# Performance work log

Hardware: AMD Instinct MI355X
Metric: run time of the kernel (lower is better)

Reference implementation:

```python
import jax, jax.numpy as jnp
import numpy as np

J = 1.0          # coupling constant
PT_PERIOD = 4    # parallel-tempering exchange every PT_PERIOD sweeps


def setup_inputs() -> dict:
    key = jax.random.key(0)
    k1, k2 = jax.random.split(key)
    B, C, L = 32, 16, 256
    # temperatures across the Ising critical region, sorted ascending
    T = jnp.sort(1.5 + 2.0 * jax.random.uniform(k1, (B,), dtype=jnp.float32))
    # spins stored as {0,1} ints; converted to +/-1 inside reference
    spins = jax.random.randint(k2, (B, C, L, L), 0, 2).astype(jnp.int32)
    return {"T": T, "spins": spins, "n_sweeps": 16}


def _neighbor_sum(s):
    # periodic 4-neighbor sum, shape preserved [B,C,L,L]
    return (jnp.roll(s, 1, -1) + jnp.roll(s, -1, -1)
            + jnp.roll(s, 1, -2) + jnp.roll(s, -1, -2))


def _energy(s):
    # total Ising energy per chain: -J * sum_<ij> s_i s_j  -> [B, C]
    return -J * jnp.sum(s * (jnp.roll(s, -1, -1) + jnp.roll(s, -1, -2)), axis=(-1, -2))


def reference(T, spins, n_sweeps):
    B, C, L, _ = spins.shape
    s = spins.astype(jnp.float32) * 2.0 - 1.0          # +/-1 spins
    ii = jnp.arange(L)
    parity = (ii[:, None] + ii[None, :]) % 2            # [L,L] checkerboard
    Tb = T[:, None, None, None]                         # [B,1,1,1]
    beta = 1.0 / T                                      # [B]
    base_key = jax.random.key(42)

    def half_sweep(s, key, color):
        dE = 2.0 * J * s * _neighbor_sum(s)             # local energy change on flip
        u = jax.random.uniform(key, s.shape, dtype=jnp.float32)
        acc = u < jnp.exp(-dE / Tb)                     # Metropolis accept
        mask = (parity == color)                        # update one sub-lattice only
        return jnp.where(mask & acc, -s, s)

    def pt_swap(s, key, pair_parity):
        # attempt swaps between adjacent temperatures (b, b+1) with given pair parity
        E = _energy(s)                                  # [B, C]
        d = (beta[:-1] - beta[1:])[:, None] * (E[:-1] - E[1:])   # [B-1, C]
        u = jax.random.uniform(key, (B - 1, C), dtype=jnp.float32)
        pair_mask = (jnp.arange(B - 1) % 2) == pair_parity
        acc = (u < jnp.exp(d)) & pair_mask[:, None]     # [B-1, C] non-overlapping
        swap_next = jnp.concatenate([acc, jnp.zeros((1, C), bool)], 0)  # swap b<->b+1
        swap_prev = jnp.concatenate([jnp.zeros((1, C), bool), acc], 0)
        s_next = jnp.roll(s, -1, axis=0)
        s_prev = jnp.roll(s, 1, axis=0)
        swn = swap_next[:, :, None, None]
        swp = swap_prev[:, :, None, None]
        return jnp.where(swn, s_next, jnp.where(swp, s_prev, s))

    def sweep(s, t):
        kb = jax.random.fold_in(base_key, t)
        k1, k2, k3 = jax.random.split(kb, 3)
        s = half_sweep(s, k1, 0)   # black sub-lattice
        s = half_sweep(s, k2, 1)   # white sub-lattice
        do_pt = (t % PT_PERIOD) == (PT_PERIOD - 1)
        s = jax.lax.cond(do_pt,
                         lambda s_: pt_swap(s_, k3, (t // PT_PERIOD) % 2),
                         lambda s_: s_, s)
        return s, None

    s, _ = jax.lax.scan(sweep, s, jnp.arange(n_sweeps))
    return s, _energy(s)
```

## Files before the change

### kernel.cpp

```cpp
#include <hip/hip_runtime.h>
#include <stdint.h>


#define BB 32
#define CC 16
#define PLANE 65536
#define NSITE (BB * CC * PLANE)
#define NPAIR ((BB - 1) * CC)
#define HSTRIP 64
#define ROWS_LD 69

__host__ __device__ __forceinline__ void tf2x32(uint32_t k0, uint32_t k1,
                                                uint32_t c0, uint32_t c1,
                                                uint32_t& o0, uint32_t& o1) {
  uint32_t ks2 = k0 ^ k1 ^ 0x1BD11BDAu;
  uint32_t x0 = c0 + k0;
  uint32_t x1 = c1 + k1;
#define TF_ROT(r) { x0 += x1; x1 = (x1 << (r)) | (x1 >> (32 - (r))); x1 ^= x0; }
  TF_ROT(13) TF_ROT(15) TF_ROT(26) TF_ROT(6)
  x0 += k1;  x1 += ks2 + 1u;
  TF_ROT(17) TF_ROT(29) TF_ROT(16) TF_ROT(24)
  x0 += ks2; x1 += k0 + 2u;
  TF_ROT(13) TF_ROT(15) TF_ROT(26) TF_ROT(6)
  x0 += k0;  x1 += k1 + 3u;
  TF_ROT(17) TF_ROT(29) TF_ROT(16) TF_ROT(24)
  x0 += k1;  x1 += ks2 + 4u;
  TF_ROT(13) TF_ROT(15) TF_ROT(26) TF_ROT(6)
  x0 += ks2; x1 += k0 + 5u;
#undef TF_ROT
  o0 = x0; o1 = x1;
}

__device__ __forceinline__ float u01(uint32_t bits) {
  return __uint_as_float((bits >> 9) | 0x3f800000u) - 1.0f;
}

__global__ __launch_bounds__(256) void init8_k(const int* __restrict__ spins,
                                               uint8_t* __restrict__ s) {
  int i = blockIdx.x * 256 + threadIdx.x;
  int4 v = ((const int4*)spins)[i];
  uint32_t o = ((uint32_t)(uint8_t)(int8_t)(2 * v.x - 1))
             | ((uint32_t)(uint8_t)(int8_t)(2 * v.y - 1) << 8)
             | ((uint32_t)(uint8_t)(int8_t)(2 * v.z - 1) << 16)
             | ((uint32_t)(uint8_t)(int8_t)(2 * v.w - 1) << 24);
  ((uint32_t*)s)[i] = o;
}

__global__ void prep_k(const float* __restrict__ T,
                       uint32_t* __restrict__ M4, uint32_t* __restrict__ M8) {
  int b = threadIdx.x;
  if (b < BB) {
    float t = T[b];
    float th4 = (float)exp((double)((-4.0f) / t));
    float th8 = (float)exp((double)((-8.0f) / t));
    M4[b] = (uint32_t)ceil((double)th4 * 8388608.0);
    M8[b] = (uint32_t)ceil((double)th8 * 8388608.0);
  }
}

__device__ __forceinline__ void process_row(uint32_t* tile32, int j, int y0,
                                            int lane, uint32_t bcbase,
                                            int color, uint32_t k0, uint32_t k1,
                                            uint32_t M4b, uint32_t M8b) {
  int gy = (y0 - 2 + j) & 255;
  uint32_t rowkey = bcbase + ((uint32_t)gy << 8) + (uint32_t)(lane << 2);
  int base = j * 64 + lane;
  uint32_t cur = tile32[base];
  uint32_t up  = tile32[base - 64];
  uint32_t dn  = tile32[base + 64];
  uint32_t pw  = tile32[j * 64 + ((lane + 63) & 63)];
  uint32_t nw  = tile32[j * 64 + ((lane + 1) & 63)];
  uint32_t lft = (cur << 8) | (pw >> 24);
  uint32_t rgt = (cur >> 8) | (nw << 24);
  uint32_t kd = ((up >> 1) & 0x01010101u) + ((dn >> 1) & 0x01010101u)
              + ((lft >> 1) & 0x01010101u) + ((rgt >> 1) & 0x01010101u);
  int p = (gy + color) & 1;
  uint32_t flip = 0;
#pragma unroll
  for (int sIt = 0; sIt < 2; ++sIt) {
    int i = p + 2 * sIt;
    uint32_t kdi = (kd >> (8 * i)) & 0xFFu;
    uint32_t si  = (cur >> (8 * i + 1)) & 1u;
    uint32_t m   = si ? (4u - kdi) : kdi;
    bool accept = true;
    if (m < 2u) {
      uint32_t h0, h1;
      tf2x32(k0, k1, 0u, rowkey + (uint32_t)i, h0, h1);
      uint32_t n = (h0 ^ h1) >> 9;
      accept = n < (m == 1u ? M4b : M8b);
    }
    if (accept) flip |= (0xFEu << (8 * i));
  }
  tile32[base] = cur ^ flip;
}

__global__ __launch_bounds__(256) void sweep_k(
    const uint8_t* __restrict__ src, uint8_t* __restrict__ dst,
    const uint32_t* __restrict__ M4, const uint32_t* __restrict__ M8,
    uint32_t kA0, uint32_t kA1, uint32_t kB0, uint32_t kB1,
    int t, const int* __restrict__ nsw, float* __restrict__ Estrip, int doE) {
  __shared__ __align__(16) uint32_t tile32[ROWS_LD * 64];
  __shared__ int red[4];
  int tid   = threadIdx.x;
  int bc    = blockIdx.x >> 2;
  int strip = blockIdx.x & 3;
  int y0    = strip << 6;
  int b     = bc >> 4;
  uint32_t bcbase = (uint32_t)bc << 16;
  const uint8_t* sp = src + ((size_t)bc << 16);
  uint8_t*       dp = dst + ((size_t)bc << 16);
  bool active = (t < *nsw);
  uint32_t M4b = M4[b], M8b = M8[b];

  for (int it = 0; it < 5; ++it) {
    int i = it * 256 + tid;
    if (i < ROWS_LD * 16) {
      int gy = (y0 - 2 + (i >> 4)) & 255;
      ((uint4*)tile32)[i] = *(const uint4*)(sp + (gy << 8) + ((i & 15) << 4));
    }
  }
  __syncthreads();

  int w = tid >> 6, lane = tid & 63;

  if (active) {
    for (int j = 1 + w; j < 68; j += 4)
      process_row(tile32, j, y0, lane, bcbase, 0, kA0, kA1, M4b, M8b);
  }
  __syncthreads();
  if (active) {
    for (int j = 2 + w; j < 67; j += 4)
      process_row(tile32, j, y0, lane, bcbase, 1, kB0, kB1, M4b, M8b);
  }
  __syncthreads();

  for (int it = 0; it < 4; ++it) {
    int i = it * 256 + tid;
    int gy = y0 + (i >> 4);
    *(uint4*)(dp + (gy << 8) + ((i & 15) << 4)) = ((uint4*)tile32)[32 + i];
  }

  if (doE) {
    int acc = 0;
#pragma unroll 4
    for (int q = 0; q < 16; ++q) {
      int j = 2 + w + 4 * q;
      uint32_t cur = tile32[j * 64 + lane];
      uint32_t nxt = tile32[j * 64 + ((lane + 1) & 63)];
      uint32_t dwn = tile32[j * 64 + 64 + lane];
      uint32_t rsh = (cur >> 8) | (nxt << 24);
      int d = __builtin_popcount((cur ^ rsh) & 0x02020202u)
            + __builtin_popcount((cur ^ dwn) & 0x02020202u);
      acc += 8 - 2 * d;
    }
    for (int off = 32; off > 0; off >>= 1) acc += __shfl_down(acc, off, 64);
    if (lane == 0) red[w] = acc;
    __syncthreads();
    if (tid == 0)
      Estrip[blockIdx.x] = (float)(red[0] + red[1] + red[2] + red[3]);
  }
}

__global__ void pt_decide_k(const float* __restrict__ Estrip,
                            const float* __restrict__ T,
                            float* __restrict__ Eplane,
                            uint32_t k0, uint32_t k1, int pair_parity,
                            int* __restrict__ accf, int t,
                            const int* __restrict__ nsw) {
  int tid = threadIdx.x;
  float e = Estrip[tid * 4] + Estrip[tid * 4 + 1]
          + Estrip[tid * 4 + 2] + Estrip[tid * 4 + 3];
  Eplane[tid] = -e;
  __syncthreads();
  if (tid < NPAIR) {
    if (t >= *nsw) { accf[tid] = 0; return; }
    int b = tid >> 4;
    float d = (1.0f / T[b] - 1.0f / T[b + 1]) * (Eplane[tid] - Eplane[tid + 16]);
    uint32_t h0, h1;
    tf2x32(k0, k1, 0u, (uint32_t)tid, h0, h1);
    float u = u01(h0 ^ h1);
    float th = (float)exp((double)d);
    accf[tid] = (u < th) && ((b & 1) == pair_parity);
  }
}

__global__ __launch_bounds__(256) void pt_swap8_k(uint8_t* __restrict__ s,
                                                  const int* __restrict__ accf) {
  int pc = blockIdx.x;
  if (!accf[pc]) return;
  uint4* p0 = (uint4*)(s + ((size_t)pc << 16));
  uint4* p1 = p0 + (CC * PLANE / 16);
  for (int j = threadIdx.x; j < PLANE / 16; j += 256) {
    uint4 a0 = p0[j], a1 = p1[j];
    p0[j] = a1; p1[j] = a0;
  }
}

__global__ void final_eout_k(const float* __restrict__ Eplane,
                             const int* __restrict__ accf,
                             float* __restrict__ Eout) {
  int tid = threadIdx.x;
  int b = tid >> 4;
  float e = Eplane[tid];
  if (b < 31 && accf[tid])      e = Eplane[tid + 16];
  if (b > 0  && accf[tid - 16]) e = Eplane[tid - 16];
  Eout[tid] = e;
}

__global__ __launch_bounds__(256) void expand_k(const int8_t* __restrict__ st,
                                                float* __restrict__ out,
                                                int lo, int cnt4) {
  int i = blockIdx.x * 256 + threadIdx.x;
  if (i >= cnt4) return;
  uint32_t v = *(const uint32_t*)(st + lo + 4 * i);
  float4 o;
  o.x = (float)(int8_t)(v);
  o.y = (float)(int8_t)(v >> 8);
  o.z = (float)(int8_t)(v >> 16);
  o.w = (float)(int8_t)(v >> 24);
  ((float4*)out)[(lo >> 2) + i] = o;
}

__global__ __launch_bounds__(256) void expand_head_k(const int8_t* __restrict__ st,
                                                     float* __restrict__ out) {
  uint32_t r[8];
  int t = threadIdx.x;
  for (int u = 0; u < 8; ++u) r[u] = *(const uint32_t*)(st + t * 32 + 4 * u);
  __syncthreads();
  for (int u = 0; u < 8; ++u) {
    uint32_t v = r[u];
    float4 o;
    o.x = (float)(int8_t)(v);
    o.y = (float)(int8_t)(v >> 8);
    o.z = (float)(int8_t)(v >> 16);
    o.w = (float)(int8_t)(v >> 24);
    ((float4*)out)[t * 8 + u] = o;
  }
}

extern "C" void kernel_launch(void* const* d_in, const int* in_sizes, int n_in,
                              void* d_out, int out_size, void* d_ws, size_t ws_size,
                              hipStream_t stream) {
  (void)in_sizes; (void)n_in; (void)out_size; (void)ws_size;
  const float* T    = (const float*)d_in[0];
  const int*  spins = (const int*)d_in[1];
  const int*  nsw   = (const int*)d_in[2];

  uint8_t* buf0 = (uint8_t*)d_out;
  uint8_t* buf1 = buf0 + NSITE;
  float*   outf = (float*)d_out;
  float*   Eout = outf + NSITE;

  float*    Estrip = (float*)d_ws;
  float*    Eplane = Estrip + 2048;
  uint32_t* M4     = (uint32_t*)(Eplane + 512);
  uint32_t* M8     = M4 + BB;
  int*      accf   = (int*)(M8 + BB);

  init8_k<<<NSITE / 1024, 256, 0, stream>>>(spins, buf0);
  prep_k<<<1, 64, 0, stream>>>(T, M4, M8);

  for (int t = 0; t < 16; ++t) {
    uint32_t kb0, kb1;
    tf2x32(0u, 42u, 0u, (uint32_t)t, kb0, kb1);
    uint32_t k1a, k1b, k2a, k2b, k3a, k3b;
    tf2x32(kb0, kb1, 0u, 0u, k1a, k1b);
    tf2x32(kb0, kb1, 0u, 1u, k2a, k2b);
    tf2x32(kb0, kb1, 0u, 2u, k3a, k3b);

    uint8_t* src = (t & 1) ? buf1 : buf0;
    uint8_t* dst = (t & 1) ? buf0 : buf1;
    int doE = ((t & 3) == 3);
    sweep_k<<<BB * CC * 4, 256, 0, stream>>>(src, dst, M4, M8,
                                             k1a, k1b, k2a, k2b, t, nsw,
                                             Estrip, doE);
    if (doE) {
      pt_decide_k<<<1, 512, 0, stream>>>(Estrip, T, Eplane, k3a, k3b,
                                         (t >> 2) & 1, accf, t, nsw);
      pt_swap8_k<<<NPAIR, 256, 0, stream>>>(buf0, accf);
    }
  }

  final_eout_k<<<1, 512, 0, stream>>>(Eplane, accf, Eout);

  for (int lo = NSITE / 4; lo >= 8192; lo >>= 2) {
    int cnt4 = (lo * 3) / 4;
    expand_k<<<(cnt4 + 255) / 256, 256, 0, stream>>>((int8_t*)buf0, outf, lo, cnt4);
  }
  expand_head_k<<<1, 256, 0, stream>>>((int8_t*)buf0, outf);
}
```

Baseline: 1.676 ms.

## Fuse four sweeps per launch with whole 256x256 plane resident in LDS

Each block now loads an entire 64KB int8 plane into shared memory and runs all four sweeps between parallel-tempering exchanges in place, with periodic wraparound handled inside LDS. This removes the per-sweep global round trip, the halo reloads and the ping-pong buffer, and cuts the sweep launches from sixteen to four. The energy reduction is folded into the same kernel, so the strip-energy buffer goes away. The cost is 512 blocks of 1024 threads each using 64KB of LDS, which lowers occupancy and leaves fewer blocks than the earlier 2048, and there are extra block-wide barriers between color phases.

Measured after the change: 1.520 ms. 1.1x faster.

```diff
diff --git a/kernel.cpp b/kernel.cpp
--- a/kernel.cpp
+++ b/kernel.cpp
@@ -7,8 +7,6 @@
 #define PLANE 65536
 #define NSITE (BB * CC * PLANE)
 #define NPAIR ((BB - 1) * CC)
-#define HSTRIP 64
-#define ROWS_LD 69
 
 __host__ __device__ __forceinline__ void tf2x32(uint32_t k0, uint32_t k1,
                                                 uint32_t c0, uint32_t c1,
@@ -58,130 +56,124 @@
   }
 }
 
-__device__ __forceinline__ void process_row(uint32_t* tile32, int j, int y0,
-                                            int lane, uint32_t bcbase,
-                                            int color, uint32_t k0, uint32_t k1,
-                                            uint32_t M4b, uint32_t M8b) {
-  int gy = (y0 - 2 + j) & 255;
-  uint32_t rowkey = bcbase + ((uint32_t)gy << 8) + (uint32_t)(lane << 2);
-  int base = j * 64 + lane;
-  uint32_t cur = tile32[base];
-  uint32_t up  = tile32[base - 64];
-  uint32_t dn  = tile32[base + 64];
-  uint32_t pw  = tile32[j * 64 + ((lane + 63) & 63)];
-  uint32_t nw  = tile32[j * 64 + ((lane + 1) & 63)];
-  uint32_t lft = (cur << 8) | (pw >> 24);
-  uint32_t rgt = (cur >> 8) | (nw << 24);
-  uint32_t kd = ((up >> 1) & 0x01010101u) + ((dn >> 1) & 0x01010101u)
-              + ((lft >> 1) & 0x01010101u) + ((rgt >> 1) & 0x01010101u);
-  int p = (gy + color) & 1;
-  uint32_t flip = 0;
+__device__ __forceinline__ void do_color(uint32_t* __restrict__ tile,
+    int w, int lane, uint32_t bcbase, int color,
+    uint32_t k0, uint32_t k1, uint32_t M4b, uint32_t M8b) {
+  int lm = (lane + 63) & 63, lp = (lane + 1) & 63;
+#pragma unroll 4
+  for (int j = w; j < 256; j += 16) {
+    int rb = j << 6;
+    uint32_t cur = tile[rb + lane];
+    uint32_t up  = tile[(((j + 255) & 255) << 6) + lane];
+    uint32_t dn  = tile[(((j + 1) & 255) << 6) + lane];
+    uint32_t pw  = tile[rb + lm];
+    uint32_t nw  = tile[rb + lp];
+    uint32_t lft = (cur << 8) | (pw >> 24);
+    uint32_t rgt = (cur >> 8) | (nw << 24);
+    uint32_t kd = ((up >> 1) & 0x01010101u) + ((dn >> 1) & 0x01010101u)
+                + ((lft >> 1) & 0x01010101u) + ((rgt >> 1) & 0x01010101u);
+    int p = (j + color) & 1;
+    uint32_t rowkey = bcbase + ((uint32_t)j << 8)
+                    + (uint32_t)(lane << 2) + (uint32_t)p;
+    uint32_t flip = 0;
+    {
+      uint32_t kdi = (kd >> (8 * p)) & 0xFFu;
+      uint32_t si  = (cur >> (8 * p + 1)) & 1u;
+      uint32_t m   = si ? (4u - kdi) : kdi;
+      bool a = true;
+      if (m < 2u) {
+        uint32_t h0, h1;
+        tf2x32(k0, k1, 0u, rowkey, h0, h1);
+        a = ((h0 ^ h1) >> 9) < (m ? M4b : M8b);
+      }
+      if (a) flip |= 0xFEu << (8 * p);
+    }
+    {
+      uint32_t kdi = (kd >> (8 * p + 16)) & 0xFFu;
+      uint32_t si  = (cur >> (8 * p + 17)) & 1u;
+      uint32_t m   = si ? (4u - kdi) : kdi;
+      bool a = true;
+      if (m < 2u) {
+        uint32_t h0, h1;
+        tf2x32(k0, k1, 0u, rowkey + 2u, h0, h1);
+        a = ((h0 ^ h1) >> 9) < (m ? M4b : M8b);
+      }
+      if (a) flip |= 0xFE0000u << (8 * p);
+    }
+    tile[rb + lane] = cur ^ flip;
+  }
+}
+
+__global__ __launch_bounds__(1024) void sweep4_k(
+    uint8_t* __restrict__ sg,
+    const uint32_t* __restrict__ M4, const uint32_t* __restrict__ M8,
+    uint4 kS0, uint4 kS1, uint4 kS2, uint4 kS3,
+    int tbase, const int* __restrict__ nsw, float* __restrict__ Eplane) {
+  __shared__ uint32_t tile[16384];
+  int tid = threadIdx.x;
+  int bc  = blockIdx.x;
+  int b   = bc >> 4;
+  uint32_t bcbase = (uint32_t)bc << 16;
+  uint32_t* gp = (uint32_t*)(sg + ((size_t)bc << 16));
+  uint32_t M4b = M4[b], M8b = M8[b];
+  int nswv = *nsw;
+
+  for (int i = tid; i < 4096; i += 1024)
+    ((uint4*)tile)[i] = ((const uint4*)gp)[i];
+  __syncthreads();
+
+  int w = tid >> 6, lane = tid & 63;
+  uint4 keys[4] = {kS0, kS1, kS2, kS3};
 #pragma unroll
-  for (int sIt = 0; sIt < 2; ++sIt) {
-    int i = p + 2 * sIt;
-    uint32_t kdi = (kd >> (8 * i)) & 0xFFu;
-    uint32_t si  = (cur >> (8 * i + 1)) & 1u;
-    uint32_t m   = si ? (4u - kdi) : kdi;
-    bool accept = true;
-    if (m < 2u) {
-      uint32_t h0, h1;
-      tf2x32(k0, k1, 0u, rowkey + (uint32_t)i, h0, h1);
-      uint32_t n = (h0 ^ h1) >> 9;
-      accept = n < (m == 1u ? M4b : M8b);
-    }
-    if (accept) flip |= (0xFEu << (8 * i));
-  }
-  tile32[base] = cur ^ flip;
-}
-
-__global__ __launch_bounds__(256) void sweep_k(
-    const uint8_t* __restrict__ src, uint8_t* __restrict__ dst,
-    const uint32_t* __restrict__ M4, const uint32_t* __restrict__ M8,
-    uint32_t kA0, uint32_t kA1, uint32_t kB0, uint32_t kB1,
-    int t, const int* __restrict__ nsw, float* __restrict__ Estrip, int doE) {
-  __shared__ __align__(16) uint32_t tile32[ROWS_LD * 64];
-  __shared__ int red[4];
-  int tid   = threadIdx.x;
-  int bc    = blockIdx.x >> 2;
-  int strip = blockIdx.x & 3;
-  int y0    = strip << 6;
-  int b     = bc >> 4;
-  uint32_t bcbase = (uint32_t)bc << 16;
-  const uint8_t* sp = src + ((size_t)bc << 16);
-  uint8_t*       dp = dst + ((size_t)bc << 16);
-  bool active = (t < *nsw);
-  uint32_t M4b = M4[b], M8b = M8[b];
-
-  for (int it = 0; it < 5; ++it) {
-    int i = it * 256 + tid;
-    if (i < ROWS_LD * 16) {
-      int gy = (y0 - 2 + (i >> 4)) & 255;
-      ((uint4*)tile32)[i] = *(const uint4*)(sp + (gy << 8) + ((i & 15) << 4));
-    }
-  }
-  __syncthreads();
-
-  int w = tid >> 6, lane = tid & 63;
-
-  if (active) {
-    for (int j = 1 + w; j < 68; j += 4)
-      process_row(tile32, j, y0, lane, bcbase, 0, kA0, kA1, M4b, M8b);
-  }
-  __syncthreads();
-  if (active) {
-    for (int j = 2 + w; j < 67; j += 4)
-      process_row(tile32, j, y0, lane, bcbase, 1, kB0, kB1, M4b, M8b);
-  }
-  __syncthreads();
-
-  for (int it = 0; it < 4; ++it) {
-    int i = it * 256 + tid;
-    int gy = y0 + (i >> 4);
-    *(uint4*)(dp + (gy << 8) + ((i & 15) << 4)) = ((uint4*)tile32)[32 + i];
-  }
-
-  if (doE) {
-    int acc = 0;
-#pragma unroll 4
-    for (int q = 0; q < 16; ++q) {
-      int j = 2 + w + 4 * q;
-      uint32_t cur = tile32[j * 64 + lane];
-      uint32_t nxt = tile32[j * 64 + ((lane + 1) & 63)];
-      uint32_t dwn = tile32[j * 64 + 64 + lane];
-      uint32_t rsh = (cur >> 8) | (nxt << 24);
-      int d = __builtin_popcount((cur ^ rsh) & 0x02020202u)
-            + __builtin_popcount((cur ^ dwn) & 0x02020202u);
-      acc += 8 - 2 * d;
-    }
-    for (int off = 32; off > 0; off >>= 1) acc += __shfl_down(acc, off, 64);
-    if (lane == 0) red[w] = acc;
-    __syncthreads();
-    if (tid == 0)
-      Estrip[blockIdx.x] = (float)(red[0] + red[1] + red[2] + red[3]);
-  }
-}
-
-__global__ void pt_decide_k(const float* __restrict__ Estrip,
+  for (int ss = 0; ss < 4; ++ss) {
+    if (tbase + ss < nswv) {
+      do_color(tile, w, lane, bcbase, 0, keys[ss].x, keys[ss].y, M4b, M8b);
+      __syncthreads();
+      do_color(tile, w, lane, bcbase, 1, keys[ss].z, keys[ss].w, M4b, M8b);
+      __syncthreads();
+    }
+  }
+
+  int acc = 0;
+  for (int j = w; j < 256; j += 16) {
+    uint32_t cur = tile[(j << 6) + lane];
+    uint32_t nxt = tile[(j << 6) + ((lane + 1) & 63)];
+    uint32_t dwn = tile[(((j + 1) & 255) << 6) + lane];
+    uint32_t rsh = (cur >> 8) | (nxt << 24);
+    int d = __builtin_popcount((cur ^ rsh) & 0x02020202u)
+          + __builtin_popcount((cur ^ dwn) & 0x02020202u);
+    acc += 8 - 2 * d;
+  }
+
+  for (int i = tid; i < 4096; i += 1024)
+    ((uint4*)gp)[i] = ((uint4*)tile)[i];
+  __syncthreads();
+
+  for (int off = 32; off > 0; off >>= 1) acc += __shfl_down(acc, off, 64);
+  if (lane == 0) tile[w] = (uint32_t)acc;
+  __syncthreads();
+  if (tid == 0) {
+    int tot = 0;
+    for (int i = 0; i < 16; ++i) tot += (int)tile[i];
+    Eplane[bc] = -(float)tot;
+  }
+}
+
+__global__ void pt_decide_k(const float* __restrict__ Eplane,
                             const float* __restrict__ T,
-                            float* __restrict__ Eplane,
                             uint32_t k0, uint32_t k1, int pair_parity,
                             int* __restrict__ accf, int t,
                             const int* __restrict__ nsw) {
   int tid = threadIdx.x;
-  float e = Estrip[tid * 4] + Estrip[tid * 4 + 1]
-          + Estrip[tid * 4 + 2] + Estrip[tid * 4 + 3];
-  Eplane[tid] = -e;
-  __syncthreads();
-  if (tid < NPAIR) {
-    if (t >= *nsw) { accf[tid] = 0; return; }
-    int b = tid >> 4;
-    float d = (1.0f / T[b] - 1.0f / T[b + 1]) * (Eplane[tid] - Eplane[tid + 16]);
-    uint32_t h0, h1;
-    tf2x32(k0, k1, 0u, (uint32_t)tid, h0, h1);
-    float u = u01(h0 ^ h1);
-    float th = (float)exp((double)d);
-    accf[tid] = (u < th) && ((b & 1) == pair_parity);
-  }
+  if (tid >= NPAIR) return;
+  if (t >= *nsw) { accf[tid] = 0; return; }
+  int b = tid >> 4;
+  float d = (1.0f / T[b] - 1.0f / T[b + 1]) * (Eplane[tid] - Eplane[tid + 16]);
+  uint32_t h0, h1;
+  tf2x32(k0, k1, 0u, (uint32_t)tid, h0, h1);
+  float u = u01(h0 ^ h1);
+  float th = (float)exp((double)d);
+  accf[tid] = (u < th) && ((b & 1) == pair_parity);
 }
 
 __global__ __launch_bounds__(256) void pt_swap8_k(uint8_t* __restrict__ s,
@@ -247,12 +239,10 @@
   const int*  nsw   = (const int*)d_in[2];
 
   uint8_t* buf0 = (uint8_t*)d_out;
-  uint8_t* buf1 = buf0 + NSITE;
   float*   outf = (float*)d_out;
   float*   Eout = outf + NSITE;
 
-  float*    Estrip = (float*)d_ws;
-  float*    Eplane = Estrip + 2048;
+  float*    Eplane = (float*)d_ws;
   uint32_t* M4     = (uint32_t*)(Eplane + 512);
   uint32_t* M8     = M4 + BB;
   int*      accf   = (int*)(M8 + BB);
@@ -260,25 +250,23 @@
   init8_k<<<NSITE / 1024, 256, 0, stream>>>(spins, buf0);
   prep_k<<<1, 64, 0, stream>>>(T, M4, M8);
 
-  for (int t = 0; t < 16; ++t) {
-    uint32_t kb0, kb1;
-    tf2x32(0u, 42u, 0u, (uint32_t)t, kb0, kb1);
-    uint32_t k1a, k1b, k2a, k2b, k3a, k3b;
-    tf2x32(kb0, kb1, 0u, 0u, k1a, k1b);
-    tf2x32(kb0, kb1, 0u, 1u, k2a, k2b);
-    tf2x32(kb0, kb1, 0u, 2u, k3a, k3b);
-
-    uint8_t* src = (t & 1) ? buf1 : buf0;
-    uint8_t* dst = (t & 1) ? buf0 : buf1;
-    int doE = ((t & 3) == 3);
-    sweep_k<<<BB * CC * 4, 256, 0, stream>>>(src, dst, M4, M8,
-                                             k1a, k1b, k2a, k2b, t, nsw,
-                                             Estrip, doE);
-    if (doE) {
-      pt_decide_k<<<1, 512, 0, stream>>>(Estrip, T, Eplane, k3a, k3b,
-                                         (t >> 2) & 1, accf, t, nsw);
-      pt_swap8_k<<<NPAIR, 256, 0, stream>>>(buf0, accf);
-    }
+  for (int g = 0; g < 4; ++g) {
+    uint4 kS[4];
+    uint32_t k3a = 0, k3b = 0;
+    for (int i = 0; i < 4; ++i) {
+      int t = 4 * g + i;
+      uint32_t kb0, kb1;
+      tf2x32(0u, 42u, 0u, (uint32_t)t, kb0, kb1);
+      tf2x32(kb0, kb1, 0u, 0u, kS[i].x, kS[i].y);
+      tf2x32(kb0, kb1, 0u, 1u, kS[i].z, kS[i].w);
+      if (i == 3) tf2x32(kb0, kb1, 0u, 2u, k3a, k3b);
+    }
+    sweep4_k<<<BB * CC, 1024, 0, stream>>>(buf0, M4, M8,
+                                           kS[0], kS[1], kS[2], kS[3],
+                                           4 * g, nsw, Eplane);
+    pt_decide_k<<<1, 512, 0, stream>>>(Eplane, T, k3a, k3b, g & 1,
+                                       accf, 4 * g + 3, nsw);
+    pt_swap8_k<<<NPAIR, 256, 0, stream>>>(buf0, accf);
   }
 
   final_eout_k<<<1, 512, 0, stream>>>(Eplane, accf, Eout);
```
